# Performance work log

Hardware: AMD Instinct MI355X
Metric: run time of the kernel (lower is better)

## Reference

```python
import jax, jax.numpy as jnp
import numpy as np

IN_FEATURES = 212445
NODE_SIZES = [IN_FEATURES, 65536, 16384, 128]
N_CLASSES = 20
BATCH = 32


def setup_inputs() -> dict:
    key = jax.random.key(0)
    ks = jax.random.split(key, 16)
    inp = {
        "x": jax.random.normal(ks[0], (BATCH, IN_FEATURES), dtype=jnp.float32),
        "W0": jax.random.normal(ks[1], (32, 1), dtype=jnp.float32) * 0.1,
        "b0": jax.random.normal(ks[2], (32,), dtype=jnp.float32) * 0.1,
        "W1": jax.random.normal(ks[3], (64, 32), dtype=jnp.float32) * 0.1,
        "b1": jax.random.normal(ks[4], (64,), dtype=jnp.float32) * 0.1,
        "W2": jax.random.normal(ks[5], (128, 64), dtype=jnp.float32) * 0.1,
        "b2": jax.random.normal(ks[6], (128,), dtype=jnp.float32) * 0.1,
        "fc_w": jax.random.normal(ks[7], (N_CLASSES, 128 * 128), dtype=jnp.float32) * 0.01,
        "fc_b": jax.random.normal(ks[8], (N_CLASSES,), dtype=jnp.float32) * 0.01,
        # random-tree adjacency: each input node has one parent output node
        "parent0": jax.random.randint(ks[9], (NODE_SIZES[0],), 0, NODE_SIZES[1], dtype=jnp.int32),
        "parent1": jax.random.randint(ks[10], (NODE_SIZES[1],), 0, NODE_SIZES[2], dtype=jnp.int32),
        "parent2": jax.random.randint(ks[11], (NODE_SIZES[2],), 0, NODE_SIZES[3], dtype=jnp.int32),
    }
    return inp


def _fgl(z, parent, n_out, W, b):
    """FGL layer: tree-adjacency reduction over nodes + channel mix.
    z: [N, C_in, n_in] -> [N, C_out, n_out]
    """
    N, C, n_in = z.shape
    # segment-sum reduce input nodes into their parent output node
    zt = jnp.moveaxis(z, 2, 0).reshape(n_in, N * C)          # [n_in, N*C]
    s = jax.ops.segment_sum(zt, parent, num_segments=n_out)  # [n_out, N*C]
    s = jnp.moveaxis(s.reshape(n_out, N, C), 0, 2)           # [N, C_in, n_out]
    # channel mixing (weight-normed linear over channels, shared across nodes)
    return jnp.einsum("oc,ncj->noj", W, s) + b[None, :, None]


def reference(x, W0, b0, W1, b1, W2, b2, fc_w, fc_b, parent0, parent1, parent2):
    N = x.shape[0]
    z = x[:, None, :]                                   # [N, 1, in_features]
    z = _fgl(z, parent0, NODE_SIZES[1], W0, b0)         # [N, 32, 65536]
    z = _fgl(z, parent1, NODE_SIZES[2], W1, b1)         # [N, 64, 16384]
    z = _fgl(z, parent2, NODE_SIZES[3], W2, b2)         # [N, 128, 128]
    logits = z.reshape(N, -1) @ fc_w.T + fc_b           # [N, n_classes]
    return logits
```

## Files before the change

### kernel.cpp

```cpp
#include <hip/hip_runtime.h>

#define IN_FEATURES 212445
#define N1 65536
#define N2 16384
#define NCLS 20
#define BATCH 32
#define HIST_BLOCKS 32
#define MCHUNK 1024
#define MBLOCKS ((IN_FEATURES + MCHUNK - 1) / MCHUNK)
#define TCHUNK 4096
#define TCHUNKS ((IN_FEATURES + TCHUNK - 1) / TCHUNK)


__global__ __launch_bounds__(256) void k_setup(
    const float* __restrict__ W0, const float* __restrict__ b0,
    const float* __restrict__ W1, const float* __restrict__ b1,
    const float* __restrict__ W2,
    const int* __restrict__ p0, const int* __restrict__ p1,
    const int* __restrict__ p2,
    float* __restrict__ t3, int* __restrict__ hist,
    float* __restrict__ u2, float* __restrict__ v2, float* __restrict__ w2,
    int* __restrict__ midx)
{
    int t = threadIdx.x;
    int b = blockIdx.x;
    if (b == 0) {
        __shared__ float su1[64], sv1[64];
        if (t < 64) {
            float a = 0.f, bb = 0.f;
            for (int c = 0; c < 32; ++c) {
                float w = W1[t * 32 + c];
                a  += w * W0[c];
                bb += w * b0[c];
            }
            su1[t] = a; sv1[t] = bb;
        }
        __syncthreads();
        if (t < 128) {
            float a = 0.f, bb = 0.f, c = 0.f;
            for (int j = 0; j < 64; ++j) {
                float w = W2[t * 64 + j];
                a  += w * su1[j];
                bb += w * sv1[j];
                c  += w * b1[j];
            }
            u2[t] = a; v2[t] = bb; w2[t] = c;
        }
    } else if (b == 1) {
        for (int s = t; s < BATCH * 128; s += 256) t3[s] = 0.f;
    } else if (b < 2 + HIST_BLOCKS) {
        __shared__ int hA[128], hB[128];
        if (t < 128) { hA[t] = 0; hB[t] = 0; }
        __syncthreads();
        const int total = N1 + N2;
        const int stride = HIST_BLOCKS * 256;
        for (int idx = (b - 2) * 256 + t; idx < total; idx += stride) {
            if (idx < N1) atomicAdd(&hA[p2[p1[idx]]], 1);
            else          atomicAdd(&hB[p2[idx - N1]], 1);
        }
        __syncthreads();
        hist[(b - 2) * 256 + t] = (t < 128) ? hA[t] : hB[t - 128];
    } else {
        int mb = b - (2 + HIST_BLOCKS);
        int base = mb * MCHUNK;
        #pragma unroll
        for (int u = 0; u < MCHUNK / 256; ++u) {
            int i = base + u * 256 + t;
            if (i < IN_FEATURES) midx[i] = p2[p1[p0[i]]];
        }
    }
}

__global__ __launch_bounds__(256) void k_t3(
    const float* __restrict__ x, const int* __restrict__ midx,
    float* __restrict__ t3)
{
    __shared__ float hist[4 * 128];
    int t = threadIdx.x;
    for (int s = t; s < 512; s += 256) hist[s] = 0.f;
    __syncthreads();

    int row   = blockIdx.x & 31;
    int chunk = blockIdx.x >> 5;
    int base  = chunk * TCHUNK;
    const float* xr = x + (size_t)row * IN_FEATURES;
    float* hw = hist + (t >> 6) * 128;

    if (base + TCHUNK <= IN_FEATURES) {
        for (int k = 0; k < TCHUNK / 1024; ++k) {
            float v[4]; int mi[4];
            #pragma unroll
            for (int u = 0; u < 4; ++u) {
                int i = base + (k * 4 + u) * 256 + t;
                v[u]  = xr[i];
                mi[u] = midx[i];
            }
            #pragma unroll
            for (int u = 0; u < 4; ++u)
                atomicAdd(&hw[mi[u]], v[u]);
        }
    } else {
        for (int i = base + t; i < IN_FEATURES; i += 256)
            atomicAdd(&hw[midx[i]], xr[i]);
    }
    __syncthreads();
    if (t < 128) {
        float s = hist[t] + hist[128 + t] + hist[256 + t] + hist[384 + t];
        atomicAdd(&t3[row * 128 + t], s);
    }
}

__global__ __launch_bounds__(256) void k_final(
    const float* __restrict__ fc_w, const float* __restrict__ fc_b,
    const float* __restrict__ b2,
    const float* __restrict__ u2, const float* __restrict__ v2,
    const float* __restrict__ w2,
    const int* __restrict__ hist, const float* __restrict__ t3,
    float* __restrict__ out)
{
    __shared__ float su[128], sv[128], sw[128], sb[128];
    __shared__ float sA[128];
    __shared__ float pA[256], pV[256], pW[256], pB[256];
    __shared__ float red[256];
    __shared__ float st3[BATCH * 129];
    __shared__ float sconst;
    int t = threadIdx.x;
    int m = t & 127, h = t >> 7;
    int cls = blockIdx.x;

    if (h == 0) { su[m] = u2[m]; sv[m] = v2[m]; sw[m] = w2[m]; sb[m] = b2[m]; }
    for (int s = t; s < BATCH * 128; s += 256)
        st3[(s >> 7) * 129 + (s & 127)] = t3[s];
    __syncthreads();

    const float* fw = fc_w + cls * 16384 + m;
    float Sa = 0.f, Sv = 0.f, Sw = 0.f, Sb = 0.f;
    #pragma unroll 8
    for (int o = h * 64; o < h * 64 + 64; ++o) {
        float wv = fw[o * 128];
        Sa += wv * su[o]; Sv += wv * sv[o]; Sw += wv * sw[o]; Sb += wv * sb[o];
    }
    pA[t] = Sa; pV[t] = Sv; pW[t] = Sw; pB[t] = Sb;
    __syncthreads();
    if (h == 0) {
        Sa = pA[m] + pA[128 + m]; Sv = pV[m] + pV[128 + m];
        Sw = pW[m] + pW[128 + m]; Sb = pB[m] + pB[128 + m];
        int c2 = 0, cn2 = 0;
        #pragma unroll
        for (int hb = 0; hb < HIST_BLOCKS; ++hb) {
            c2  += hist[hb * 256 + m];
            cn2 += hist[hb * 256 + 128 + m];
        }
        sA[m] = Sa;
        red[m] = (float)c2 * Sv + (float)cn2 * Sw + Sb;
    }
    __syncthreads();
    for (int s2 = 64; s2 > 0; s2 >>= 1) {
        if (t < s2) red[t] += red[t + s2];
        __syncthreads();
    }
    if (t == 0) sconst = red[0] + fc_b[cls];
    __syncthreads();

    int n = t >> 3, oc = t & 7;
    const float* tr = st3 + n * 129 + oc * 16;
    const float* ar = sA + oc * 16;
    float s = 0.f;
    #pragma unroll
    for (int k = 0; k < 16; ++k) s += ar[k] * tr[k];
    red[t] = s;
    __syncthreads();
    if (oc == 0) {
        float tot = sconst;
        #pragma unroll
        for (int k = 0; k < 8; ++k) tot += red[t + k];
        out[n * NCLS + cls] = tot;
    }
}

extern "C" void kernel_launch(void* const* d_in, const int* in_sizes, int n_in,
                              void* d_out, int out_size, void* d_ws, size_t ws_size,
                              hipStream_t stream)
{
    const float* x    = (const float*)d_in[0];
    const float* W0   = (const float*)d_in[1];
    const float* b0   = (const float*)d_in[2];
    const float* W1   = (const float*)d_in[3];
    const float* b1   = (const float*)d_in[4];
    const float* W2   = (const float*)d_in[5];
    const float* b2   = (const float*)d_in[6];
    const float* fc_w = (const float*)d_in[7];
    const float* fc_b = (const float*)d_in[8];
    const int*   p0   = (const int*)d_in[9];
    const int*   p1   = (const int*)d_in[10];
    const int*   p2   = (const int*)d_in[11];

    char* ws = (char*)d_ws;
    float* t3   = (float*)(ws + 0);
    int*   hist = (int*)(ws + 16384);
    float* u2   = (float*)(ws + 49152);
    float* v2   = (float*)(ws + 49664);
    float* w2   = (float*)(ws + 50176);
    int*   midx = (int*)(ws + 51200);

    k_setup<<<2 + HIST_BLOCKS + MBLOCKS, 256, 0, stream>>>(
        W0, b0, W1, b1, W2, p0, p1, p2, t3, hist, u2, v2, w2, midx);
    k_t3<<<BATCH * TCHUNKS, 256, 0, stream>>>(x, midx, t3);
    k_final<<<NCLS, 256, 0, stream>>>(fc_w, fc_b, b2, u2, v2, w2, hist, t3,
                                      (float*)d_out);
}
```

Baseline: 137.9 us.

## Flatten x into float4 chunks spanning rows and move fc_w folding into setup

```diff
diff --git a/kernel.cpp b/kernel.cpp
--- a/kernel.cpp
+++ b/kernel.cpp
@@ -8,24 +8,33 @@
 #define HIST_BLOCKS 32
 #define MCHUNK 1024
 #define MBLOCKS ((IN_FEATURES + MCHUNK - 1) / MCHUNK)
-#define TCHUNK 4096
-#define TCHUNKS ((IN_FEATURES + TCHUNK - 1) / TCHUNK)
+#define TOTF (BATCH * IN_FEATURES)
+#define TOTF4 (TOTF / 4)
+#define CF4 2048
+#define NT3B ((TOTF4 + CF4 - 1) / CF4)
 
 
 __global__ __launch_bounds__(256) void k_setup(
     const float* __restrict__ W0, const float* __restrict__ b0,
     const float* __restrict__ W1, const float* __restrict__ b1,
-    const float* __restrict__ W2,
+    const float* __restrict__ W2, const float* __restrict__ b2,
+    const float* __restrict__ fc_w,
     const int* __restrict__ p0, const int* __restrict__ p1,
     const int* __restrict__ p2,
     float* __restrict__ t3, int* __restrict__ hist,
-    float* __restrict__ u2, float* __restrict__ v2, float* __restrict__ w2,
+    float* __restrict__ Sa, float* __restrict__ Sv,
+    float* __restrict__ Sw, float* __restrict__ Sb,
     int* __restrict__ midx)
 {
     int t = threadIdx.x;
     int b = blockIdx.x;
     if (b == 0) {
+        for (int s = t; s < BATCH * 128; s += 256) t3[s] = 0.f;
+    } else if (b < 1 + NCLS) {
+        int cls = b - 1;
         __shared__ float su1[64], sv1[64];
+        __shared__ float lu[128], lv[128], lw[128], lb[128];
+        __shared__ float qA[256], qV[256], qW[256], qB[256];
         if (t < 64) {
             float a = 0.f, bb = 0.f;
             for (int c = 0; c < 32; ++c) {
@@ -37,31 +46,50 @@
         }
         __syncthreads();
         if (t < 128) {
-            float a = 0.f, bb = 0.f, c = 0.f;
+            float a = 0.f, bb = 0.f, cc = 0.f;
             for (int j = 0; j < 64; ++j) {
                 float w = W2[t * 64 + j];
                 a  += w * su1[j];
                 bb += w * sv1[j];
-                c  += w * b1[j];
-            }
-            u2[t] = a; v2[t] = bb; w2[t] = c;
-        }
-    } else if (b == 1) {
-        for (int s = t; s < BATCH * 128; s += 256) t3[s] = 0.f;
-    } else if (b < 2 + HIST_BLOCKS) {
+                cc += w * b1[j];
+            }
+            lu[t] = a; lv[t] = bb; lw[t] = cc; lb[t] = b2[t];
+        }
+        __syncthreads();
+        int m = t & 127, h = t >> 7;
+        const float* fw = fc_w + cls * 16384 + m;
+        float A = 0.f, V = 0.f, Wt = 0.f, Bt = 0.f;
+        #pragma unroll 16
+        for (int o = h * 64; o < h * 64 + 64; ++o) {
+            float wv = fw[o * 128];
+            A  += wv * lu[o];
+            V  += wv * lv[o];
+            Wt += wv * lw[o];
+            Bt += wv * lb[o];
+        }
+        qA[t] = A; qV[t] = V; qW[t] = Wt; qB[t] = Bt;
+        __syncthreads();
+        if (h == 0) {
+            Sa[cls * 128 + m] = qA[m] + qA[128 + m];
+            Sv[cls * 128 + m] = qV[m] + qV[128 + m];
+            Sw[cls * 128 + m] = qW[m] + qW[128 + m];
+            Sb[cls * 128 + m] = qB[m] + qB[128 + m];
+        }
+    } else if (b < 1 + NCLS + HIST_BLOCKS) {
         __shared__ int hA[128], hB[128];
         if (t < 128) { hA[t] = 0; hB[t] = 0; }
         __syncthreads();
         const int total = N1 + N2;
         const int stride = HIST_BLOCKS * 256;
-        for (int idx = (b - 2) * 256 + t; idx < total; idx += stride) {
+        int hb = b - (1 + NCLS);
+        for (int idx = hb * 256 + t; idx < total; idx += stride) {
             if (idx < N1) atomicAdd(&hA[p2[p1[idx]]], 1);
             else          atomicAdd(&hB[p2[idx - N1]], 1);
         }
         __syncthreads();
-        hist[(b - 2) * 256 + t] = (t < 128) ? hA[t] : hB[t - 128];
+        hist[hb * 256 + t] = (t < 128) ? hA[t] : hB[t - 128];
     } else {
-        int mb = b - (2 + HIST_BLOCKS);
+        int mb = b - (1 + NCLS + HIST_BLOCKS);
         int base = mb * MCHUNK;
         #pragma unroll
         for (int u = 0; u < MCHUNK / 256; ++u) {
@@ -75,85 +103,103 @@
     const float* __restrict__ x, const int* __restrict__ midx,
     float* __restrict__ t3)
 {
-    __shared__ float hist[4 * 128];
+    __shared__ float hist[4 * 256];
     int t = threadIdx.x;
-    for (int s = t; s < 512; s += 256) hist[s] = 0.f;
-    __syncthreads();
-
-    int row   = blockIdx.x & 31;
-    int chunk = blockIdx.x >> 5;
-    int base  = chunk * TCHUNK;
-    const float* xr = x + (size_t)row * IN_FEATURES;
-    float* hw = hist + (t >> 6) * 128;
-
-    if (base + TCHUNK <= IN_FEATURES) {
-        for (int k = 0; k < TCHUNK / 1024; ++k) {
-            float v[4]; int mi[4];
+    #pragma unroll
+    for (int s = t; s < 1024; s += 256) hist[s] = 0.f;
+    __syncthreads();
+
+    int b = blockIdx.x;
+    int f0 = b * (CF4 * 4);
+    int row0 = f0 / IN_FEATURES;
+    int rb = row0 * IN_FEATURES;
+    float* hw = hist + (t >> 6) * 256;
+    const float4* x4 = (const float4*)x;
+    int base4 = b * CF4 + t;
+
+    if (b != NT3B - 1) {
+        for (int kk = 0; kk < 4; ++kk) {
+            int fA = base4 + (2 * kk) * 256;
+            int fB = base4 + (2 * kk + 1) * 256;
+            float4 vA = x4[fA];
+            float4 vB = x4[fB];
+            int lA = fA * 4 - rb;
+            int lB = fB * 4 - rb;
+            int mi[8], sl[8];
             #pragma unroll
-            for (int u = 0; u < 4; ++u) {
-                int i = base + (k * 4 + u) * 256 + t;
-                v[u]  = xr[i];
-                mi[u] = midx[i];
+            for (int e = 0; e < 4; ++e) {
+                int l = lA + e; int sg = (l >= IN_FEATURES);
+                sl[e] = sg; mi[e] = midx[sg ? l - IN_FEATURES : l];
             }
             #pragma unroll
-            for (int u = 0; u < 4; ++u)
-                atomicAdd(&hw[mi[u]], v[u]);
+            for (int e = 0; e < 4; ++e) {
+                int l = lB + e; int sg = (l >= IN_FEATURES);
+                sl[4 + e] = sg; mi[4 + e] = midx[sg ? l - IN_FEATURES : l];
+            }
+            atomicAdd(&hw[sl[0] * 128 + mi[0]], vA.x);
+            atomicAdd(&hw[sl[1] * 128 + mi[1]], vA.y);
+            atomicAdd(&hw[sl[2] * 128 + mi[2]], vA.z);
+            atomicAdd(&hw[sl[3] * 128 + mi[3]], vA.w);
+            atomicAdd(&hw[sl[4] * 128 + mi[4]], vB.x);
+            atomicAdd(&hw[sl[5] * 128 + mi[5]], vB.y);
+            atomicAdd(&hw[sl[6] * 128 + mi[6]], vB.z);
+            atomicAdd(&hw[sl[7] * 128 + mi[7]], vB.w);
         }
     } else {
-        for (int i = base + t; i < IN_FEATURES; i += 256)
-            atomicAdd(&hw[midx[i]], xr[i]);
+        for (int kk = 0; kk < 8; ++kk) {
+            int f4 = base4 + kk * 256;
+            if (f4 < TOTF4) {
+                float4 v = x4[f4];
+                int l0 = f4 * 4 - rb;
+                float vv[4] = {v.x, v.y, v.z, v.w};
+                #pragma unroll
+                for (int e = 0; e < 4; ++e) {
+                    int l = l0 + e; int sg = (l >= IN_FEATURES);
+                    atomicAdd(&hw[sg * 128 + midx[sg ? l - IN_FEATURES : l]], vv[e]);
+                }
+            }
+        }
     }
     __syncthreads();
     if (t < 128) {
-        float s = hist[t] + hist[128 + t] + hist[256 + t] + hist[384 + t];
-        atomicAdd(&t3[row * 128 + t], s);
+        float s0 = hist[t] + hist[256 + t] + hist[512 + t] + hist[768 + t];
+        atomicAdd(&t3[row0 * 128 + t], s0);
+        int bnd = rb + IN_FEATURES;
+        int fend = f0 + CF4 * 4; if (fend > TOTF) fend = TOTF;
+        if (row0 + 1 < BATCH && bnd < fend) {
+            float s1 = hist[128 + t] + hist[384 + t] + hist[640 + t] + hist[896 + t];
+            atomicAdd(&t3[(row0 + 1) * 128 + t], s1);
+        }
     }
 }
 
 __global__ __launch_bounds__(256) void k_final(
-    const float* __restrict__ fc_w, const float* __restrict__ fc_b,
-    const float* __restrict__ b2,
-    const float* __restrict__ u2, const float* __restrict__ v2,
-    const float* __restrict__ w2,
+    const float* __restrict__ fc_b,
+    const float* __restrict__ Sa, const float* __restrict__ Sv,
+    const float* __restrict__ Sw, const float* __restrict__ Sb,
     const int* __restrict__ hist, const float* __restrict__ t3,
     float* __restrict__ out)
 {
-    __shared__ float su[128], sv[128], sw[128], sb[128];
-    __shared__ float sA[128];
-    __shared__ float pA[256], pV[256], pW[256], pB[256];
-    __shared__ float red[256];
+    __shared__ float sA[128], red[128], r2[256];
     __shared__ float st3[BATCH * 129];
     __shared__ float sconst;
     int t = threadIdx.x;
-    int m = t & 127, h = t >> 7;
     int cls = blockIdx.x;
 
-    if (h == 0) { su[m] = u2[m]; sv[m] = v2[m]; sw[m] = w2[m]; sb[m] = b2[m]; }
-    for (int s = t; s < BATCH * 128; s += 256)
-        st3[(s >> 7) * 129 + (s & 127)] = t3[s];
-    __syncthreads();
-
-    const float* fw = fc_w + cls * 16384 + m;
-    float Sa = 0.f, Sv = 0.f, Sw = 0.f, Sb = 0.f;
-    #pragma unroll 8
-    for (int o = h * 64; o < h * 64 + 64; ++o) {
-        float wv = fw[o * 128];
-        Sa += wv * su[o]; Sv += wv * sv[o]; Sw += wv * sw[o]; Sb += wv * sb[o];
-    }
-    pA[t] = Sa; pV[t] = Sv; pW[t] = Sw; pB[t] = Sb;
-    __syncthreads();
-    if (h == 0) {
-        Sa = pA[m] + pA[128 + m]; Sv = pV[m] + pV[128 + m];
-        Sw = pW[m] + pW[128 + m]; Sb = pB[m] + pB[128 + m];
+    if (t < 128) {
         int c2 = 0, cn2 = 0;
         #pragma unroll
         for (int hb = 0; hb < HIST_BLOCKS; ++hb) {
-            c2  += hist[hb * 256 + m];
-            cn2 += hist[hb * 256 + 128 + m];
-        }
-        sA[m] = Sa;
-        red[m] = (float)c2 * Sv + (float)cn2 * Sw + Sb;
-    }
+            c2  += hist[hb * 256 + t];
+            cn2 += hist[hb * 256 + 128 + t];
+        }
+        sA[t]  = Sa[cls * 128 + t];
+        red[t] = (float)c2 * Sv[cls * 128 + t]
+               + (float)cn2 * Sw[cls * 128 + t]
+               + Sb[cls * 128 + t];
+    }
+    for (int s = t; s < BATCH * 128; s += 256)
+        st3[(s >> 7) * 129 + (s & 127)] = t3[s];
     __syncthreads();
     for (int s2 = 64; s2 > 0; s2 >>= 1) {
         if (t < s2) red[t] += red[t + s2];
@@ -168,12 +214,12 @@
     float s = 0.f;
     #pragma unroll
     for (int k = 0; k < 16; ++k) s += ar[k] * tr[k];
-    red[t] = s;
+    r2[t] = s;
     __syncthreads();
     if (oc == 0) {
         float tot = sconst;
         #pragma unroll
-        for (int k = 0; k < 8; ++k) tot += red[t + k];
+        for (int k = 0; k < 8; ++k) tot += r2[t + k];
         out[n * NCLS + cls] = tot;
     }
 }
@@ -198,14 +244,15 @@
     char* ws = (char*)d_ws;
     float* t3   = (float*)(ws + 0);
     int*   hist = (int*)(ws + 16384);
-    float* u2   = (float*)(ws + 49152);
-    float* v2   = (float*)(ws + 49664);
-    float* w2   = (float*)(ws + 50176);
-    int*   midx = (int*)(ws + 51200);
-
-    k_setup<<<2 + HIST_BLOCKS + MBLOCKS, 256, 0, stream>>>(
-        W0, b0, W1, b1, W2, p0, p1, p2, t3, hist, u2, v2, w2, midx);
-    k_t3<<<BATCH * TCHUNKS, 256, 0, stream>>>(x, midx, t3);
-    k_final<<<NCLS, 256, 0, stream>>>(fc_w, fc_b, b2, u2, v2, w2, hist, t3,
+    float* Sa   = (float*)(ws + 49152);
+    float* Sv   = (float*)(ws + 59392);
+    float* Sw   = (float*)(ws + 69632);
+    float* Sb   = (float*)(ws + 79872);
+    int*   midx = (int*)(ws + 90112);
+
+    k_setup<<<1 + NCLS + HIST_BLOCKS + MBLOCKS, 256, 0, stream>>>(
+        W0, b0, W1, b1, W2, b2, fc_w, p0, p1, p2, t3, hist, Sa, Sv, Sw, Sb, midx);
+    k_t3<<<NT3B, 256, 0, stream>>>(x, midx, t3);
+    k_final<<<NCLS, 256, 0, stream>>>(fc_b, Sa, Sv, Sw, Sb, hist, t3,
                                       (float*)d_out);
 }
```

Measured after the change: 139.8 us. About the same (+1.3%).
